# Performance work log

Measured on AMD Instinct MI355X. Metric: run time of the kernel, lower is better.

Reference implementation:

```python
import jax, jax.numpy as jnp
import numpy as np

EPS = 1e-5
B, C, H, W, K = 16, 512, 64, 64, 32


def setup_inputs() -> dict:
    key = jax.random.key(0)
    ks = jax.random.split(key, 6)
    std = 1.0 / float(np.sqrt(K * C))
    return {
        "x": jax.random.normal(ks[0], (B, C, H, W), jnp.float32),
        "conv_w": jax.random.normal(ks[1], (C, C), jnp.float32) * (1.0 / np.sqrt(C)),
        "bn2_g": jnp.ones((C,), jnp.float32),
        "bn2_b": jnp.zeros((C,), jnp.float32),
        "bn2_m": jnp.zeros((C,), jnp.float32),
        "bn2_v": jnp.ones((C,), jnp.float32),
        "codewords": jax.random.uniform(ks[2], (K, C), jnp.float32, -std, std),
        "scale": jax.random.uniform(ks[3], (K,), jnp.float32, -1.0, 0.0),
        "bn1_g": jnp.ones((K,), jnp.float32),
        "bn1_b": jnp.zeros((K,), jnp.float32),
        "bn1_m": jnp.zeros((K,), jnp.float32),
        "bn1_v": jnp.ones((K,), jnp.float32),
        "fc_w": jax.random.normal(ks[4], (C, C), jnp.float32) * (1.0 / np.sqrt(C)),
        "fc_b": jnp.zeros((C,), jnp.float32),
    }


def reference(x, conv_w, bn2_g, bn2_b, bn2_m, bn2_v, codewords, scale,
              bn1_g, bn1_b, bn1_m, bn1_v, fc_w, fc_b):
    b, c, h, w = x.shape
    k = codewords.shape[0]
    # encoding_project: 1x1 conv (no bias) + BatchNorm2d (inference) + ReLU
    proj = jnp.einsum('oc,bchw->bohw', conv_w, x)
    s2 = (jax.lax.rsqrt(bn2_v + EPS) * bn2_g)[None, :, None, None]
    proj = jax.nn.relu((proj - bn2_m[None, :, None, None]) * s2 + bn2_b[None, :, None, None])
    # Encoding: scaled-L2 softmax assignment + residual aggregation
    feats = proj.reshape(b, c, h * w).transpose(0, 2, 1)          # (B, N, C)
    x2 = jnp.sum(feats * feats, axis=-1)                          # (B, N)
    c2 = jnp.sum(codewords * codewords, axis=-1)                  # (K,)
    xc = jnp.einsum('bnc,kc->bnk', feats, codewords)              # (B, N, K)
    dist = scale[None, None, :] * (x2[..., None] - 2.0 * xc + c2[None, None, :])
    assign = jax.nn.softmax(dist, axis=2)                         # (B, N, K)
    # sum_n w[b,n,k] * (x[b,n,c] - c[k,c])  without materializing (B,N,K,C)
    encoded = (jnp.einsum('bnk,bnc->bkc', assign, feats)
               - jnp.einsum('bnk,kc->bkc', assign, codewords))    # (B, K, C)
    # BatchNorm1d over num_codes (inference) + ReLU
    s1 = (jax.lax.rsqrt(bn1_v + EPS) * bn1_g)[None, :, None]
    encoded = jax.nn.relu((encoded - bn1_m[None, :, None]) * s1 + bn1_b[None, :, None])
    encoding_feat = jnp.mean(encoded, axis=1)                     # (B, C)
    # fc -> sigmoid gate, residual relu
    gamma = jax.nn.sigmoid(encoding_feat @ fc_w.T + fc_b)         # (B, C)
    output = jax.nn.relu(x + x * gamma[:, :, None, None])
    return (encoding_feat, output)
```

## Files before the change

kernel.cpp:

```cpp
#include <hip/hip_runtime.h>
#include <hip/hip_bf16.h>

#define BB   16
#define CC   512
#define HWN  4096
#define KK   32
#define EPSF 1e-5f

typedef short bf16x8 __attribute__((ext_vector_type(8)));
typedef float f32x4  __attribute__((ext_vector_type(4)));

#define MFMA16 __builtin_amdgcn_mfma_f32_16x16x32_bf16

#define GLD16(g, l) __builtin_amdgcn_global_load_lds(                          \
    (const __attribute__((address_space(1))) void*)(g),                        \
    (__attribute__((address_space(3))) void*)(l), 16, 0, 0)

#define EADDR(o, n) ((o) * 136 + (((((n) >> 3) ^ (((o) >> 3) & 15))) << 3) + ((n) & 7))

static __device__ __forceinline__ unsigned short f2b(float f) {
    unsigned u = __builtin_bit_cast(unsigned, f);
    unsigned r = (u + 0x7FFFu + ((u >> 16) & 1u)) >> 16;
    return (unsigned short)r;
}

__global__ __launch_bounds__(256) void k_prep(const float* __restrict__ W,
                                              const float* __restrict__ cw,
                                              const float* __restrict__ scale,
                                              const float* __restrict__ g1,
                                              const float* __restrict__ b1,
                                              const float* __restrict__ m1,
                                              const float* __restrict__ v1,
                                              unsigned short* __restrict__ Wb,
                                              unsigned short* __restrict__ cwb,
                                              float* __restrict__ sc2,
                                              float* __restrict__ s1,
                                              float* __restrict__ t1) {
    int bid = blockIdx.x, t = threadIdx.x;
    if (bid < 256) {
        int i = (bid * 256 + t) * 4;
        float4 v = *(const float4*)(W + i);
        uint2 p;
        p.x = (unsigned)f2b(v.x) | ((unsigned)f2b(v.y) << 16);
        p.y = (unsigned)f2b(v.z) | ((unsigned)f2b(v.w) << 16);
        *(uint2*)(Wb + i) = p;
    } else if (bid < 272) {
        int i = ((bid - 256) * 256 + t) * 4;
        float4 v = *(const float4*)(cw + i);
        uint2 p;
        p.x = (unsigned)f2b(v.x) | ((unsigned)f2b(v.y) << 16);
        p.y = (unsigned)f2b(v.z) | ((unsigned)f2b(v.w) << 16);
        *(uint2*)(cwb + i) = p;
    } else {
        int k = t >> 3, l8 = t & 7;
        const float* row = cw + k * CC + l8 * 64;
        float s = 0.f;
#pragma unroll
        for (int i = 0; i < 16; i++) {
            float4 c4 = *(const float4*)(row + i * 4);
            s += c4.x * c4.x + c4.y * c4.y + c4.z * c4.z + c4.w * c4.w;
        }
        s += __shfl_xor(s, 1); s += __shfl_xor(s, 2); s += __shfl_xor(s, 4);
        if (l8 == 0) sc2[k] = scale[k] * s;
        if (t < KK) {
            float sv = rsqrtf(v1[t] + EPSF) * g1[t];
            s1[t] = sv;
            t1[t] = b1[t] - m1[t] * sv;
        }
    }
}

__global__ __launch_bounds__(256) void k_transpose(const float* __restrict__ x,
                                                   unsigned short* __restrict__ xT) {
    __shared__ float tile[64][65];
    int bid = blockIdx.x;
    int b   = bid >> 9;
    int rem = bid & 511;
    int c0  = (rem >> 6) * 64;
    int n0  = (rem & 63) * 64;
    int t = threadIdx.x;
#pragma unroll
    for (int p = 0; p < 4; p++) {
        int s = p * 256 + t;
        int row = s >> 4, col = (s & 15) * 4;
        float4 v = *(const float4*)(x + (size_t)(b * CC + c0 + row) * HWN + n0 + col);
        tile[row][col]     = v.x;
        tile[row][col + 1] = v.y;
        tile[row][col + 2] = v.z;
        tile[row][col + 3] = v.w;
    }
    __syncthreads();
    int nr = t >> 2;
    int cg = (t & 3) * 16;
    unsigned u[8];
#pragma unroll
    for (int j = 0; j < 8; j++) {
        u[j] = (unsigned)f2b(tile[cg + 2 * j][nr]) |
               ((unsigned)f2b(tile[cg + 2 * j + 1][nr]) << 16);
    }
    unsigned short* dst = xT + (size_t)(b * HWN + n0 + nr) * CC + c0 + cg;
    uint4 a; a.x = u[0]; a.y = u[1]; a.z = u[2]; a.w = u[3];
    uint4 c; c.x = u[4]; c.y = u[5]; c.z = u[6]; c.w = u[7];
    *(uint4*)(dst)     = a;
    *(uint4*)(dst + 8) = c;
}

__global__ __launch_bounds__(256) void k_conv_gemm(const unsigned short* __restrict__ xT,
                                                   const unsigned short* __restrict__ Wb,
                                                   const float* __restrict__ g2,
                                                   const float* __restrict__ b2,
                                                   const float* __restrict__ m2,
                                                   const float* __restrict__ v2,
                                                   unsigned short* __restrict__ feats,
                                                   unsigned short* __restrict__ featsT,
                                                   float* __restrict__ x2) {
    __shared__ __align__(16) short lds[17408];
    int bid = blockIdx.x;
    int b   = bid >> 7;
    int rem = bid & 127;
    int m0  = (rem >> 2) * 128;
    int o0  = (rem & 3) * 128;
    int t = threadIdx.x, lane = t & 63, wave = t >> 6;
    int mb = (wave >> 1) * 64, ob = (wave & 1) * 64;
    int col_l = lane & 15, quad = lane >> 4;

    f32x4 zero = {0.f, 0.f, 0.f, 0.f};
    f32x4 acc[4][4];
#pragma unroll
    for (int i = 0; i < 4; i++)
#pragma unroll
        for (int j = 0; j < 4; j++) acc[i][j] = zero;

    const unsigned short* Abase = xT + (size_t)(b * HWN + m0) * CC;
    const unsigned short* Bbase = Wb + (size_t)o0 * CC;

    for (int kc = 0; kc < 8; kc++) {
        int c0 = kc * 64;
#pragma unroll
        for (int pc = 0; pc < 2; pc++) {
#pragma unroll
            for (int p = 0; p < 2; p++) {
                int sbase = p * 256 + wave * 64;
                int s = sbase + lane;
                int row = s >> 2, part = (s & 3) * 8;
                GLD16(Abase + (size_t)row * CC + c0 + pc * 32 + part,
                      (char*)lds + pc * 8192 + sbase * 16);
                GLD16(Bbase + (size_t)row * CC + c0 + pc * 32 + part,
                      (char*)lds + 16384 + pc * 8192 + sbase * 16);
            }
        }
        __syncthreads();
#pragma unroll
        for (int pc = 0; pc < 2; pc++) {
            bf16x8 af[4], bfv[4];
#pragma unroll
            for (int im = 0; im < 4; im++)
                af[im] = *(const bf16x8*)(&lds[pc * 4096 + (mb + im * 16 + col_l) * 32 + quad * 8]);
#pragma unroll
            for (int in = 0; in < 4; in++)
                bfv[in] = *(const bf16x8*)(&lds[8192 + pc * 4096 + (ob + in * 16 + col_l) * 32 + quad * 8]);
#pragma unroll
            for (int im = 0; im < 4; im++)
#pragma unroll
                for (int in = 0; in < 4; in++)
                    acc[im][in] = MFMA16(af[im], bfv[in], acc[im][in], 0, 0, 0);
        }
        __syncthreads();
    }

    float scv[4], offv[4];
#pragma unroll
    for (int in = 0; in < 4; in++) {
        int o = o0 + ob + in * 16 + col_l;
        float sv = rsqrtf(v2[o] + EPSF) * g2[o];
        scv[in]  = sv;
        offv[in] = b2[o] - m2[o] * sv;
    }
#pragma unroll
    for (int im = 0; im < 4; im++) {
        int n_l = mb + im * 16 + quad * 4;
        float vv[4][4];
#pragma unroll
        for (int in = 0; in < 4; in++)
#pragma unroll
            for (int r = 0; r < 4; r++)
                vv[in][r] = fmaxf(acc[im][in][r] * scv[in] + offv[in], 0.f);
#pragma unroll
        for (int in = 0; in < 4; in++) {
            int o_l = ob + in * 16 + col_l;
            uint2 pk;
            pk.x = (unsigned)f2b(vv[in][0]) | ((unsigned)f2b(vv[in][1]) << 16);
            pk.y = (unsigned)f2b(vv[in][2]) | ((unsigned)f2b(vv[in][3]) << 16);
            *(uint2*)(&lds[EADDR(o_l, n_l)]) = pk;
        }
#pragma unroll
        for (int r = 0; r < 4; r++) {
            float ss = vv[0][r] * vv[0][r] + vv[1][r] * vv[1][r] +
                       vv[2][r] * vv[2][r] + vv[3][r] * vv[3][r];
            ss += __shfl_xor(ss, 1); ss += __shfl_xor(ss, 2);
            ss += __shfl_xor(ss, 4); ss += __shfl_xor(ss, 8);
            if (col_l == 0) atomicAdd(&x2[b * HWN + m0 + n_l + r], ss);
        }
    }
    __syncthreads();

#pragma unroll
    for (int rr = 0; rr < 8; rr++) {
        int o = rr * 16 + (t >> 4);
        int n16 = t & 15;
        uint4 v = *(const uint4*)(&lds[EADDR(o, n16 * 8)]);
        *(uint4*)(featsT + (size_t)(b * CC + o0 + o) * HWN + m0 + n16 * 8) = v;
    }
#pragma unroll
    for (int rr = 0; rr < 8; rr++) {
        int n = rr * 16 + (t >> 4);
        int o16 = t & 15;
        unsigned u[4];
#pragma unroll
        for (int jj = 0; jj < 4; jj++) {
            unsigned short a = lds[EADDR(o16 * 8 + 2 * jj,     n)];
            unsigned short bsh = lds[EADDR(o16 * 8 + 2 * jj + 1, n)];
            u[jj] = (unsigned)a | ((unsigned)bsh << 16);
        }
        uint4 pk; pk.x = u[0]; pk.y = u[1]; pk.z = u[2]; pk.w = u[3];
        *(uint4*)(feats + (size_t)(b * HWN + m0 + n) * CC + o0 + o16 * 8) = pk;
    }
}

__global__ __launch_bounds__(256) void k_assign(const unsigned short* __restrict__ feats,
                                                const unsigned short* __restrict__ cwb,
                                                const float* __restrict__ x2,
                                                const float* __restrict__ scale,
                                                const float* __restrict__ sc2,
                                                unsigned short* __restrict__ assignT,
                                                float* __restrict__ asum) {
    __shared__ short cwl[32 * 520];
    __shared__ short fl[128 * 32];
    __shared__ float sl[KK], cl[KK];
    int bid = blockIdx.x;
    int b = bid >> 5, n0 = (bid & 31) * 128;
    int t = threadIdx.x, lane = t & 63, wave = t >> 6;
    int col_l = lane & 15, quad = lane >> 4;

#pragma unroll
    for (int p = 0; p < 8; p++) {
        int s = p * 256 + t;
        int row = s >> 6, c8 = (s & 63) * 8;
        *(uint4*)(&cwl[row * 520 + c8]) = *(const uint4*)(cwb + row * 512 + c8);
    }
    if (t < KK) { sl[t] = scale[t]; cl[t] = sc2[t]; }

    f32x4 zero = {0.f, 0.f, 0.f, 0.f};
    f32x4 acc[2][2];
    acc[0][0] = zero; acc[0][1] = zero; acc[1][0] = zero; acc[1][1] = zero;

    const unsigned short* Fbase = feats + (size_t)(b * HWN + n0) * CC;
    for (int ci = 0; ci < 16; ci++) {
        int c0 = ci * 32;
#pragma unroll
        for (int p = 0; p < 2; p++) {
            int sbase = p * 256 + wave * 64;
            int s = sbase + lane;
            GLD16(Fbase + (size_t)(s >> 2) * CC + c0 + (s & 3) * 8,
                  (char*)fl + sbase * 16);
        }
        __syncthreads();
        bf16x8 af0 = *(const bf16x8*)(&cwl[(col_l) * 520 + c0 + quad * 8]);
        bf16x8 af1 = *(const bf16x8*)(&cwl[(16 + col_l) * 520 + c0 + quad * 8]);
#pragma unroll
        for (int ct = 0; ct < 2; ct++) {
            bf16x8 bf = *(const bf16x8*)(&fl[(wave * 32 + ct * 16 + col_l) * 32 + quad * 8]);
            acc[0][ct] = MFMA16(af0, bf, acc[0][ct], 0, 0, 0);
            acc[1][ct] = MFMA16(af1, bf, acc[1][ct], 0, 0, 0);
        }
        __syncthreads();
    }

    float asw[2][4];
#pragma unroll
    for (int mk = 0; mk < 2; mk++)
#pragma unroll
        for (int r = 0; r < 4; r++) asw[mk][r] = 0.f;

#pragma unroll
    for (int ct = 0; ct < 2; ct++) {
        int n = n0 + wave * 32 + ct * 16 + col_l;
        float x2v = x2[b * HWN + n];
        float d[2][4];
        float mmax = -3.4e38f;
#pragma unroll
        for (int mk = 0; mk < 2; mk++)
#pragma unroll
            for (int r = 0; r < 4; r++) {
                int k = mk * 16 + quad * 4 + r;
                d[mk][r] = sl[k] * (x2v - 2.f * acc[mk][ct][r]) + cl[k];
                mmax = fmaxf(mmax, d[mk][r]);
            }
        mmax = fmaxf(mmax, __shfl_xor(mmax, 16));
        mmax = fmaxf(mmax, __shfl_xor(mmax, 32));
        float ssum = 0.f;
#pragma unroll
        for (int mk = 0; mk < 2; mk++)
#pragma unroll
            for (int r = 0; r < 4; r++) {
                d[mk][r] = __expf(d[mk][r] - mmax);
                ssum += d[mk][r];
            }
        ssum += __shfl_xor(ssum, 16);
        ssum += __shfl_xor(ssum, 32);
        float rinv = 1.f / ssum;
#pragma unroll
        for (int mk = 0; mk < 2; mk++)
#pragma unroll
            for (int r = 0; r < 4; r++) {
                int k = mk * 16 + quad * 4 + r;
                float a = d[mk][r] * rinv;
                assignT[(size_t)(b * KK + k) * HWN + n] = f2b(a);
                float p = a;
                p += __shfl_xor(p, 1); p += __shfl_xor(p, 2);
                p += __shfl_xor(p, 4); p += __shfl_xor(p, 8);
                asw[mk][r] += p;
            }
    }
#pragma unroll
    for (int mk = 0; mk < 2; mk++)
#pragma unroll
        for (int r = 0; r < 4; r++)
            if (col_l == 0)
                atomicAdd(&asum[b * KK + mk * 16 + quad * 4 + r], asw[mk][r]);
}

__global__ __launch_bounds__(256) void k_encode(const unsigned short* __restrict__ featsT,
                                                const unsigned short* __restrict__ assignT,
                                                float* __restrict__ enc) {
    __shared__ short Al[2][128 * 32];
    __shared__ short Bl[2][32 * 32];
    int bid = blockIdx.x;
    int b   = bid >> 5;
    int rem = bid & 31;
    int c0  = (rem >> 3) * 128;
    int ns  = rem & 7;
    int t = threadIdx.x, lane = t & 63, wave = t >> 6;
    int col_l = lane & 15, quad = lane >> 4;

    f32x4 zero = {0.f, 0.f, 0.f, 0.f};
    f32x4 acc[2][2];
    acc[0][0] = zero; acc[0][1] = zero; acc[1][0] = zero; acc[1][1] = zero;

    const unsigned short* Abase = featsT + (size_t)(b * CC + c0) * HWN;
    const unsigned short* Bbase = assignT + (size_t)(b * KK) * HWN;

    for (int it = 0; it < 8; it++) {
        int n0 = ns * 512 + it * 64;
#pragma unroll
        for (int pc = 0; pc < 2; pc++) {
#pragma unroll
            for (int p = 0; p < 2; p++) {
                int sbase = p * 256 + wave * 64;
                int s = sbase + lane;
                GLD16(Abase + (size_t)(s >> 2) * HWN + n0 + pc * 32 + (s & 3) * 8,
                      (char*)Al[pc] + sbase * 16);
            }
        }
        {
            int s = t;
            int pan = s >> 7, row = (s & 127) >> 2, part = (s & 3) * 8;
            GLD16(Bbase + (size_t)row * HWN + n0 + pan * 32 + part,
                  (char*)Bl[0] + ((wave >> 1) * 2048 + (wave & 1) * 1024) + lane * 16);
            (void)pan;
        }
        __syncthreads();
#pragma unroll
        for (int pc = 0; pc < 2; pc++) {
            bf16x8 a0 = *(const bf16x8*)(&Al[pc][(wave * 32 + col_l) * 32 + quad * 8]);
            bf16x8 a1 = *(const bf16x8*)(&Al[pc][(wave * 32 + 16 + col_l) * 32 + quad * 8]);
            bf16x8 b0 = *(const bf16x8*)(&Bl[pc][(col_l) * 32 + quad * 8]);
            bf16x8 b1 = *(const bf16x8*)(&Bl[pc][(16 + col_l) * 32 + quad * 8]);
            acc[0][0] = MFMA16(a0, b0, acc[0][0], 0, 0, 0);
            acc[0][1] = MFMA16(a0, b1, acc[0][1], 0, 0, 0);
            acc[1][0] = MFMA16(a1, b0, acc[1][0], 0, 0, 0);
            acc[1][1] = MFMA16(a1, b1, acc[1][1], 0, 0, 0);
        }
        __syncthreads();
    }
#pragma unroll
    for (int i2 = 0; i2 < 2; i2++)
#pragma unroll
        for (int ck = 0; ck < 2; ck++)
#pragma unroll
            for (int r = 0; r < 4; r++) {
                int c = c0 + wave * 32 + i2 * 16 + quad * 4 + r;
                int k = ck * 16 + col_l;
                atomicAdd(&enc[(size_t)(b * CC + c) * KK + k], acc[i2][ck][r]);
            }
}

__global__ __launch_bounds__(256) void k_efeat(const float* __restrict__ enc,
                                               const float* __restrict__ asum,
                                               const float* __restrict__ cwf,
                                               const float* __restrict__ s1,
                                               const float* __restrict__ t1,
                                               float* __restrict__ efeat) {
    __shared__ float asl[KK], s1l[KK], t1l[KK];
    int b = blockIdx.x, t = threadIdx.x;
    if (t < KK) { asl[t] = asum[b * KK + t]; s1l[t] = s1[t]; t1l[t] = t1[t]; }
    __syncthreads();
#pragma unroll
    for (int cc = 0; cc < 2; cc++) {
        int c = cc * 256 + t;
        const float* er = enc + (size_t)(b * CC + c) * KK;
        float s = 0.f;
#pragma unroll
        for (int k = 0; k < KK; k++) {
            float v = (er[k] - asl[k] * cwf[k * CC + c]) * s1l[k] + t1l[k];
            s += fmaxf(v, 0.f);
        }
        efeat[b * CC + c] = s * (1.f / 32.f);
    }
}

__global__ __launch_bounds__(256) void k_fc(const float* __restrict__ efeat,
                                            const float* __restrict__ fcw,
                                            const float* __restrict__ fcb,
                                            float* __restrict__ gamma) {
    __shared__ float ef[CC];
    int bid = blockIdx.x;
    int b  = bid >> 1;
    int o0 = (bid & 1) * 256;
    int t = threadIdx.x;
    if (t < 128) *(float4*)(&ef[t * 4]) = *(const float4*)(efeat + b * CC + t * 4);
    __syncthreads();
    int o = o0 + t;
    float a = fcb[o];
    const float* wrow = fcw + (size_t)o * CC;
#pragma unroll 4
    for (int c4 = 0; c4 < 128; c4++) {
        float4 w = *(const float4*)(wrow + c4 * 4);
        float4 e = *(const float4*)(&ef[c4 * 4]);
        a += w.x * e.x + w.y * e.y + w.z * e.z + w.w * e.w;
    }
    gamma[b * CC + o] = 1.f / (1.f + __expf(-a));
}

__global__ __launch_bounds__(256) void k_gate(const float* __restrict__ x,
                                              const float* __restrict__ gamma,
                                              float* __restrict__ out) {
    int bid = blockIdx.x;
    float g = 1.f + gamma[bid];
    const float* xr = x + ((size_t)bid << 12);
    float* orow = out + ((size_t)bid << 12);
    int t4 = threadIdx.x * 4;
#pragma unroll
    for (int u = 0; u < 4; u++) {
        float4 v = *(const float4*)(xr + u * 1024 + t4);
        v.x = fmaxf(v.x * g, 0.f);
        v.y = fmaxf(v.y * g, 0.f);
        v.z = fmaxf(v.z * g, 0.f);
        v.w = fmaxf(v.w * g, 0.f);
        *(float4*)(orow + u * 1024 + t4) = v;
    }
}

extern "C" void kernel_launch(void* const* d_in, const int* in_sizes, int n_in,
                              void* d_out, int out_size, void* d_ws, size_t ws_size,
                              hipStream_t stream) {
    const float* x      = (const float*)d_in[0];
    const float* conv_w = (const float*)d_in[1];
    const float* bn2_g  = (const float*)d_in[2];
    const float* bn2_b  = (const float*)d_in[3];
    const float* bn2_m  = (const float*)d_in[4];
    const float* bn2_v  = (const float*)d_in[5];
    const float* cw     = (const float*)d_in[6];
    const float* scale  = (const float*)d_in[7];
    const float* bn1_g  = (const float*)d_in[8];
    const float* bn1_b  = (const float*)d_in[9];
    const float* bn1_m  = (const float*)d_in[10];
    const float* bn1_v  = (const float*)d_in[11];
    const float* fc_w   = (const float*)d_in[12];
    const float* fc_b   = (const float*)d_in[13];

    float* outf = (float*)d_out;
    char* ws = (char*)d_ws;

    unsigned short* feats   = (unsigned short*)(ws);
    unsigned short* assignT = (unsigned short*)(ws + 67108864);
    unsigned short* Wb      = (unsigned short*)(ws + 71303168);
    unsigned short* cwb     = (unsigned short*)(ws + 71827456);
    float*          x2      = (float*)(ws + 71860224);
    float*          asum    = (float*)(ws + 72122368);
    float*          enc     = (float*)(ws + 72124416);
    float*          sc2     = (float*)(ws + 73172992);
    float*          s1      = (float*)(ws + 73173248);
    float*          t1      = (float*)(ws + 73173504);
    float*          gamma   = (float*)(ws + 73173760);

    unsigned short* xT     = (unsigned short*)((char*)d_out + 32768);
    unsigned short* featsT = (unsigned short*)((char*)d_out + 67141632);

    hipMemsetAsync(x2, 0, 262144 + 2048 + 1048576, stream);

    k_prep<<<273, 256, 0, stream>>>(conv_w, cw, scale, bn1_g, bn1_b, bn1_m, bn1_v,
                                    Wb, cwb, sc2, s1, t1);
    k_transpose<<<8192, 256, 0, stream>>>(x, xT);
    k_conv_gemm<<<2048, 256, 0, stream>>>(xT, Wb, bn2_g, bn2_b, bn2_m, bn2_v,
                                          feats, featsT, x2);
    k_assign<<<512, 256, 0, stream>>>(feats, cwb, x2, scale, sc2, assignT, asum);
    k_encode<<<512, 256, 0, stream>>>(featsT, assignT, enc);
    k_efeat<<<16, 256, 0, stream>>>(enc, asum, cw, s1, t1, outf);
    k_fc<<<32, 256, 0, stream>>>(outf, fc_w, fc_b, gamma);
    k_gate<<<8192, 256, 0, stream>>>(x, gamma, outf + 8192);
}
```

Before: 444.7 us.

## Double-buffer LDS loads in conv, assign and encode GEMM kernels

Converts the three MFMA GEMM loops (conv, assign, encode) to a two-stage software pipeline. The next K-slice is issued with global_load_lds into the alternate LDS buffer before computing on the current one, synchronised with explicit vmcnt waits and s_barrier. The conv kernel also remaps block IDs so adjacent blocks are spread across batches, changing cache and XCD locality. This aims to hide global load latency behind MFMA work, at the cost of more LDS per block, which may lower occupancy. The hand-counted vmcnt values make correctness fragile.

```diff
diff --git a/kernel.cpp b/kernel.cpp
--- a/kernel.cpp
+++ b/kernel.cpp
@@ -116,6 +116,7 @@
                                                    float* __restrict__ x2) {
     __shared__ __align__(16) short lds[17408];
     int bid = blockIdx.x;
+    bid = (bid & 7) * 256 + (bid >> 3);
     int b   = bid >> 7;
     int rem = bid & 127;
     int m0  = (rem >> 2) * 128;
@@ -134,39 +135,49 @@
     const unsigned short* Abase = xT + (size_t)(b * HWN + m0) * CC;
     const unsigned short* Bbase = Wb + (size_t)o0 * CC;
 
-    for (int kc = 0; kc < 8; kc++) {
-        int c0 = kc * 64;
-#pragma unroll
-        for (int pc = 0; pc < 2; pc++) {
-#pragma unroll
-            for (int p = 0; p < 2; p++) {
-                int sbase = p * 256 + wave * 64;
-                int s = sbase + lane;
-                int row = s >> 2, part = (s & 3) * 8;
-                GLD16(Abase + (size_t)row * CC + c0 + pc * 32 + part,
-                      (char*)lds + pc * 8192 + sbase * 16);
-                GLD16(Bbase + (size_t)row * CC + c0 + pc * 32 + part,
-                      (char*)lds + 16384 + pc * 8192 + sbase * 16);
-            }
-        }
-        __syncthreads();
-#pragma unroll
-        for (int pc = 0; pc < 2; pc++) {
-            bf16x8 af[4], bfv[4];
-#pragma unroll
-            for (int im = 0; im < 4; im++)
-                af[im] = *(const bf16x8*)(&lds[pc * 4096 + (mb + im * 16 + col_l) * 32 + quad * 8]);
-#pragma unroll
-            for (int in = 0; in < 4; in++)
-                bfv[in] = *(const bf16x8*)(&lds[8192 + pc * 4096 + (ob + in * 16 + col_l) * 32 + quad * 8]);
-#pragma unroll
-            for (int im = 0; im < 4; im++)
-#pragma unroll
-                for (int in = 0; in < 4; in++)
-                    acc[im][in] = MFMA16(af[im], bfv[in], acc[im][in], 0, 0, 0);
-        }
-        __syncthreads();
-    }
+#define CSTAGE(pp, bb) do {                                                   \
+    int c0_ = (pp) * 32;                                                      \
+    _Pragma("unroll")                                                         \
+    for (int p2 = 0; p2 < 2; p2++) {                                          \
+        int sbase = p2 * 256 + wave * 64;                                     \
+        int s = sbase + lane;                                                 \
+        int row = s >> 2, part = (s & 3) * 8;                                 \
+        GLD16(Abase + (size_t)row * CC + c0_ + part,                          \
+              (char*)lds + (bb) * 8192 + sbase * 16);                         \
+        GLD16(Bbase + (size_t)row * CC + c0_ + part,                          \
+              (char*)lds + 16384 + (bb) * 8192 + sbase * 16);                 \
+    } } while (0)
+
+#define CCOMP(bb) do {                                                        \
+    bf16x8 af[4], bfv[4];                                                     \
+    _Pragma("unroll")                                                         \
+    for (int im = 0; im < 4; im++)                                            \
+        af[im] = *(const bf16x8*)(&lds[(bb) * 4096 + (mb + im * 16 + col_l) * 32 + quad * 8]); \
+    _Pragma("unroll")                                                         \
+    for (int in = 0; in < 4; in++)                                            \
+        bfv[in] = *(const bf16x8*)(&lds[8192 + (bb) * 4096 + (ob + in * 16 + col_l) * 32 + quad * 8]); \
+    _Pragma("unroll")                                                         \
+    for (int im = 0; im < 4; im++)                                            \
+        _Pragma("unroll")                                                     \
+        for (int in = 0; in < 4; in++)                                        \
+            acc[im][in] = MFMA16(af[im], bfv[in], acc[im][in], 0, 0, 0);      \
+    } while (0)
+
+    CSTAGE(0, 0);
+    for (int p = 0; p < 15; p++) {
+        CSTAGE(p + 1, (p + 1) & 1);
+        asm volatile("s_waitcnt vmcnt(4)" ::: "memory");
+        __builtin_amdgcn_s_barrier();
+        asm volatile("" ::: "memory");
+        CCOMP(p & 1);
+        asm volatile("s_waitcnt lgkmcnt(0)" ::: "memory");
+        __builtin_amdgcn_s_barrier();
+    }
+    asm volatile("s_waitcnt vmcnt(0)" ::: "memory");
+    __builtin_amdgcn_s_barrier();
+    asm volatile("" ::: "memory");
+    CCOMP(1);
+    __syncthreads();
 
     float scv[4], offv[4];
 #pragma unroll
@@ -234,8 +245,7 @@
                                                 const float* __restrict__ sc2,
                                                 unsigned short* __restrict__ assignT,
                                                 float* __restrict__ asum) {
-    __shared__ short cwl[32 * 520];
-    __shared__ short fl[128 * 32];
+    __shared__ __align__(16) short lds2[24832];
     __shared__ float sl[KK], cl[KK];
     int bid = blockIdx.x;
     int b = bid >> 5, n0 = (bid & 31) * 128;
@@ -246,7 +256,7 @@
     for (int p = 0; p < 8; p++) {
         int s = p * 256 + t;
         int row = s >> 6, c8 = (s & 63) * 8;
-        *(uint4*)(&cwl[row * 520 + c8]) = *(const uint4*)(cwb + row * 512 + c8);
+        *(uint4*)(&lds2[row * 520 + c8]) = *(const uint4*)(cwb + row * 512 + c8);
     }
     if (t < KK) { sl[t] = scale[t]; cl[t] = sc2[t]; }
 
@@ -255,26 +265,44 @@
     acc[0][0] = zero; acc[0][1] = zero; acc[1][0] = zero; acc[1][1] = zero;
 
     const unsigned short* Fbase = feats + (size_t)(b * HWN + n0) * CC;
-    for (int ci = 0; ci < 16; ci++) {
-        int c0 = ci * 32;
-#pragma unroll
-        for (int p = 0; p < 2; p++) {
-            int sbase = p * 256 + wave * 64;
-            int s = sbase + lane;
-            GLD16(Fbase + (size_t)(s >> 2) * CC + c0 + (s & 3) * 8,
-                  (char*)fl + sbase * 16);
-        }
-        __syncthreads();
-        bf16x8 af0 = *(const bf16x8*)(&cwl[(col_l) * 520 + c0 + quad * 8]);
-        bf16x8 af1 = *(const bf16x8*)(&cwl[(16 + col_l) * 520 + c0 + quad * 8]);
-#pragma unroll
-        for (int ct = 0; ct < 2; ct++) {
-            bf16x8 bf = *(const bf16x8*)(&fl[(wave * 32 + ct * 16 + col_l) * 32 + quad * 8]);
-            acc[0][ct] = MFMA16(af0, bf, acc[0][ct], 0, 0, 0);
-            acc[1][ct] = MFMA16(af1, bf, acc[1][ct], 0, 0, 0);
-        }
-        __syncthreads();
-    }
+
+#define ASTAGE(ci_, bb) do {                                                  \
+    int c0_ = (ci_) * 32;                                                     \
+    _Pragma("unroll")                                                         \
+    for (int p2 = 0; p2 < 2; p2++) {                                          \
+        int sbase = p2 * 256 + wave * 64;                                     \
+        int s = sbase + lane;                                                 \
+        GLD16(Fbase + (size_t)(s >> 2) * CC + c0_ + (s & 3) * 8,              \
+              (char*)lds2 + 33280 + (bb) * 8192 + sbase * 16);                \
+    } } while (0)
+
+#define ACOMP(ci_, bb) do {                                                   \
+    int c0_ = (ci_) * 32;                                                     \
+    bf16x8 af0 = *(const bf16x8*)(&lds2[(col_l) * 520 + c0_ + quad * 8]);     \
+    bf16x8 af1 = *(const bf16x8*)(&lds2[(16 + col_l) * 520 + c0_ + quad * 8]);\
+    _Pragma("unroll")                                                         \
+    for (int ct = 0; ct < 2; ct++) {                                          \
+        bf16x8 bf = *(const bf16x8*)(&lds2[16640 + (bb) * 4096 +              \
+                     (wave * 32 + ct * 16 + col_l) * 32 + quad * 8]);         \
+        acc[0][ct] = MFMA16(af0, bf, acc[0][ct], 0, 0, 0);                    \
+        acc[1][ct] = MFMA16(af1, bf, acc[1][ct], 0, 0, 0);                    \
+    } } while (0)
+
+    ASTAGE(0, 0);
+    asm volatile("s_waitcnt lgkmcnt(0)" ::: "memory");
+    for (int ci = 0; ci < 15; ci++) {
+        ASTAGE(ci + 1, (ci + 1) & 1);
+        asm volatile("s_waitcnt vmcnt(2)" ::: "memory");
+        __builtin_amdgcn_s_barrier();
+        asm volatile("" ::: "memory");
+        ACOMP(ci, ci & 1);
+        asm volatile("s_waitcnt lgkmcnt(0)" ::: "memory");
+        __builtin_amdgcn_s_barrier();
+    }
+    asm volatile("s_waitcnt vmcnt(0)" ::: "memory");
+    __builtin_amdgcn_s_barrier();
+    asm volatile("" ::: "memory");
+    ACOMP(15, 1);
 
     float asw[2][4];
 #pragma unroll
@@ -333,8 +361,7 @@
 __global__ __launch_bounds__(256) void k_encode(const unsigned short* __restrict__ featsT,
                                                 const unsigned short* __restrict__ assignT,
                                                 float* __restrict__ enc) {
-    __shared__ short Al[2][128 * 32];
-    __shared__ short Bl[2][32 * 32];
+    __shared__ __align__(16) short lds3[20480];
     int bid = blockIdx.x;
     int b   = bid >> 5;
     int rem = bid & 31;
@@ -350,39 +377,52 @@
     const unsigned short* Abase = featsT + (size_t)(b * CC + c0) * HWN;
     const unsigned short* Bbase = assignT + (size_t)(b * KK) * HWN;
 
-    for (int it = 0; it < 8; it++) {
-        int n0 = ns * 512 + it * 64;
-#pragma unroll
-        for (int pc = 0; pc < 2; pc++) {
-#pragma unroll
-            for (int p = 0; p < 2; p++) {
-                int sbase = p * 256 + wave * 64;
-                int s = sbase + lane;
-                GLD16(Abase + (size_t)(s >> 2) * HWN + n0 + pc * 32 + (s & 3) * 8,
-                      (char*)Al[pc] + sbase * 16);
-            }
-        }
-        {
-            int s = t;
-            int pan = s >> 7, row = (s & 127) >> 2, part = (s & 3) * 8;
-            GLD16(Bbase + (size_t)row * HWN + n0 + pan * 32 + part,
-                  (char*)Bl[0] + ((wave >> 1) * 2048 + (wave & 1) * 1024) + lane * 16);
-            (void)pan;
-        }
-        __syncthreads();
-#pragma unroll
-        for (int pc = 0; pc < 2; pc++) {
-            bf16x8 a0 = *(const bf16x8*)(&Al[pc][(wave * 32 + col_l) * 32 + quad * 8]);
-            bf16x8 a1 = *(const bf16x8*)(&Al[pc][(wave * 32 + 16 + col_l) * 32 + quad * 8]);
-            bf16x8 b0 = *(const bf16x8*)(&Bl[pc][(col_l) * 32 + quad * 8]);
-            bf16x8 b1 = *(const bf16x8*)(&Bl[pc][(16 + col_l) * 32 + quad * 8]);
-            acc[0][0] = MFMA16(a0, b0, acc[0][0], 0, 0, 0);
-            acc[0][1] = MFMA16(a0, b1, acc[0][1], 0, 0, 0);
-            acc[1][0] = MFMA16(a1, b0, acc[1][0], 0, 0, 0);
-            acc[1][1] = MFMA16(a1, b1, acc[1][1], 0, 0, 0);
-        }
-        __syncthreads();
-    }
+#define ESTAGE(it_, bb) do {                                                  \
+    int n0_ = ns * 512 + (it_) * 64;                                          \
+    _Pragma("unroll")                                                         \
+    for (int pc = 0; pc < 2; pc++)                                            \
+        _Pragma("unroll")                                                     \
+        for (int p2 = 0; p2 < 2; p2++) {                                      \
+            int sbase = p2 * 256 + wave * 64;                                 \
+            int s = sbase + lane;                                             \
+            GLD16(Abase + (size_t)(s >> 2) * HWN + n0_ + pc * 32 + (s & 3) * 8, \
+                  (char*)lds3 + (bb) * 16384 + pc * 8192 + sbase * 16);       \
+        }                                                                     \
+    {   int s = t;                                                            \
+        int pan = s >> 7, row = (s & 127) >> 2, part = (s & 3) * 8;           \
+        GLD16(Bbase + (size_t)row * HWN + n0_ + pan * 32 + part,              \
+              (char*)lds3 + 32768 + (bb) * 4096 +                             \
+              ((wave >> 1) * 2048 + (wave & 1) * 1024) + lane * 16);          \
+    } } while (0)
+
+#define ECOMP(bb) do {                                                        \
+    _Pragma("unroll")                                                         \
+    for (int pc = 0; pc < 2; pc++) {                                          \
+        bf16x8 a0 = *(const bf16x8*)(&lds3[(bb) * 8192 + pc * 4096 + (wave * 32 + col_l) * 32 + quad * 8]); \
+        bf16x8 a1 = *(const bf16x8*)(&lds3[(bb) * 8192 + pc * 4096 + (wave * 32 + 16 + col_l) * 32 + quad * 8]); \
+        bf16x8 b0 = *(const bf16x8*)(&lds3[16384 + (bb) * 2048 + pc * 1024 + (col_l) * 32 + quad * 8]); \
+        bf16x8 b1 = *(const bf16x8*)(&lds3[16384 + (bb) * 2048 + pc * 1024 + (16 + col_l) * 32 + quad * 8]); \
+        acc[0][0] = MFMA16(a0, b0, acc[0][0], 0, 0, 0);                       \
+        acc[0][1] = MFMA16(a0, b1, acc[0][1], 0, 0, 0);                       \
+        acc[1][0] = MFMA16(a1, b0, acc[1][0], 0, 0, 0);                       \
+        acc[1][1] = MFMA16(a1, b1, acc[1][1], 0, 0, 0);                       \
+    } } while (0)
+
+    ESTAGE(0, 0);
+    for (int it = 0; it < 7; it++) {
+        ESTAGE(it + 1, (it + 1) & 1);
+        asm volatile("s_waitcnt vmcnt(5)" ::: "memory");
+        __builtin_amdgcn_s_barrier();
+        asm volatile("" ::: "memory");
+        ECOMP(it & 1);
+        asm volatile("s_waitcnt lgkmcnt(0)" ::: "memory");
+        __builtin_amdgcn_s_barrier();
+    }
+    asm volatile("s_waitcnt vmcnt(0)" ::: "memory");
+    __builtin_amdgcn_s_barrier();
+    asm volatile("" ::: "memory");
+    ECOMP(1);
+
 #pragma unroll
     for (int i2 = 0; i2 < 2; i2++)
 #pragma unroll
```

Result: faster. 433.6 us (-2.5%).
